# Performance work log

Hardware: AMD Instinct MI355X
Metric: run time of the kernel (lower is better)

The kernel has to match this reference:

```python
import jax, jax.numpy as jnp
import numpy as np

NU, NI, D, LAYERS, NNZ = 50000, 50000, 256, 2, 400000
N = NU + NI
LEAKY_ALPHA = 0.2  # tf.nn.leaky_relu default


def setup_inputs() -> dict:
    key = jax.random.key(0)
    ks = jax.random.split(key, 32)
    inp = {}
    inp["initial_ebs"] = jax.random.normal(ks[0], (N, D), jnp.float32) * 0.1
    for i, nm in enumerate(["W_side_u", "W_dot_u", "W_side_i", "W_dot_i"]):
        inp[nm] = jax.random.normal(ks[1 + i], (LAYERS, D, D), jnp.float32) / np.float32(np.sqrt(D))
    vi = 5
    for ent, ne in (("u", NU), ("i", NI)):
        for mat in ("LI", "L"):
            inp[f"{mat}_vals_{ent}"] = jax.random.uniform(ks[vi], (NNZ,), jnp.float32); vi += 1
            inp[f"{mat}_rows_{ent}"] = jnp.sort(jax.random.randint(ks[vi], (NNZ,), 0, ne, jnp.int32)); vi += 1
            inp[f"{mat}_cols_{ent}"] = jax.random.randint(ks[vi], (NNZ,), 0, N, jnp.int32); vi += 1
    return inp


def _spmm(rows, cols, vals, ebs, n_rows):
    # sparse [n_rows, N] @ dense [N, D] via gather + segment-sum
    return jax.ops.segment_sum(vals[:, None] * ebs[cols], rows, num_segments=n_rows)


def reference(initial_ebs, W_side_u, W_dot_u, W_side_i, W_dot_i,
              LI_vals_u, L_vals_u, LI_vals_i, L_vals_i,
              LI_rows_u, LI_cols_u, L_rows_u, L_cols_u,
              LI_rows_i, LI_cols_i, L_rows_i, L_cols_i):
    ebs = initial_ebs
    layers_ebs = []
    for l in range(LAYERS):
        # entity 'u': rows [0, NU)
        li_u = _spmm(LI_rows_u, LI_cols_u, LI_vals_u, ebs, NU)
        l_u = _spmm(L_rows_u, L_cols_u, L_vals_u, ebs, NU)
        fold_u = jax.nn.leaky_relu(li_u @ W_side_u[l] + (l_u * ebs[:NU]) @ W_dot_u[l], LEAKY_ALPHA)
        # entity 'i': rows [NU, N)
        li_i = _spmm(LI_rows_i, LI_cols_i, LI_vals_i, ebs, NI)
        l_i = _spmm(L_rows_i, L_cols_i, L_vals_i, ebs, NI)
        fold_i = jax.nn.leaky_relu(li_i @ W_side_i[l] + (l_i * ebs[NU:]) @ W_dot_i[l], LEAKY_ALPHA)
        ebs = jnp.concatenate([fold_u, fold_i], axis=0)  # [N, D]
        layers_ebs.append(ebs)
    return jnp.concatenate(layers_ebs, axis=0)  # [LAYERS*N, D]
```

## Files before the change

kernel.cpp:

```cpp
#include <hip/hip_runtime.h>

#define NUQ 50000
#define NIQ 50000
#define DQ 256
#define NTOT 100000
#define LALPHA 0.2f
#define GPE 782

typedef __attribute__((ext_vector_type(8))) __bf16 bf16x8;
typedef __attribute__((ext_vector_type(4))) float floatx4;
typedef __attribute__((ext_vector_type(8))) unsigned short ushort8;

__device__ __forceinline__ float b2f(unsigned short u) {
    unsigned int x = ((unsigned int)u) << 16;
    return __builtin_bit_cast(float, x);
}
__device__ __forceinline__ unsigned short f2b(float f) {
    unsigned int u = __builtin_bit_cast(unsigned int, f);
    u = u + 0x7FFFu + ((u >> 16) & 1u);
    return (unsigned short)(u >> 16);
}

#define GLD_LDS16(g, l)                                                        \
    __builtin_amdgcn_global_load_lds(                                          \
        (const __attribute__((address_space(1))) void*)(g),                    \
        (__attribute__((address_space(3))) void*)(l), 16, 0, 0)

__global__ __launch_bounds__(256) void build_rowptr(
    const int* __restrict__ rows, int nnz, int* __restrict__ rptr, int n_rows)
{
    int e = blockIdx.x * 256 + threadIdx.x;
    if (e > nnz) return;
    int prev = (e == 0)   ? -1     : rows[e - 1];
    int cur  = (e == nnz) ? n_rows : rows[e];
    for (int r = prev + 1; r <= cur; ++r) rptr[r] = e;
}

__global__ __launch_bounds__(256) void cvt_f32_bf16(
    const float* __restrict__ in, unsigned short* __restrict__ out, int n4)
{
    int i = blockIdx.x * 256 + threadIdx.x;
    if (i >= n4) return;
    float4 v = ((const float4*)in)[i];
    ushort4 o;
    o.x = f2b(v.x); o.y = f2b(v.y); o.z = f2b(v.z); o.w = f2b(v.w);
    ((ushort4*)out)[i] = o;
}

__global__ __launch_bounds__(256) void build_bt(
    const float* __restrict__ Ws_u, const float* __restrict__ Wd_u,
    const float* __restrict__ Ws_i, const float* __restrict__ Wd_i,
    unsigned short* __restrict__ Bt)
{
    int idx = blockIdx.x * 256 + threadIdx.x;
    int k   = idx & 511;
    int n   = (idx >> 9) & 255;
    int buf = idx >> 17;
    int l = buf >> 1, e = buf & 1;
    const float* Wside = e ? Ws_i : Ws_u;
    const float* Wdot  = e ? Wd_i : Wd_u;
    float v = (k < 256) ? Wside[((size_t)l * 256 + k)       * 256 + n]
                        : Wdot [((size_t)l * 256 + (k-256)) * 256 + n];
    Bt[idx] = f2b(v);
}

__global__ __launch_bounds__(256) void spmm_dual_v2(
    const int* __restrict__ rpA_u, const int* __restrict__ cA_u, const float* __restrict__ vA_u,
    const int* __restrict__ rpB_u, const int* __restrict__ cB_u, const float* __restrict__ vB_u,
    const int* __restrict__ rpA_i, const int* __restrict__ cA_i, const float* __restrict__ vA_i,
    const int* __restrict__ rpB_i, const int* __restrict__ cB_i, const float* __restrict__ vB_i,
    const unsigned short* __restrict__ src,
    unsigned short* __restrict__ out)
{
    const int wave = threadIdx.x >> 6;
    const int lane = threadIdx.x & 63;
    const int r    = blockIdx.x * 4 + wave;
    if (r >= NTOT) return;
    const int  isB = blockIdx.y;
    const bool isI = (r >= NUQ);
    const int  row = isI ? (r - NUQ) : r;

    const int* rptr; const int* cols; const float* vals;
    if (isB) { rptr = isI ? rpB_i : rpB_u; cols = isI ? cB_i : cB_u; vals = isI ? vB_i : vB_u; }
    else     { rptr = isI ? rpA_i : rpA_u; cols = isI ? cA_i : cA_u; vals = isI ? vA_i : vA_u; }

    const int start = rptr[row];
    const int end   = rptr[row + 1];

    const int half = lane >> 5;
    const int li   = lane & 31;

    float acc[8] = {0.f, 0.f, 0.f, 0.f, 0.f, 0.f, 0.f, 0.f};

    for (int base = start; base < end; base += 64) {
        int cnt = end - base; if (cnt > 64) cnt = 64;
        int myc = 0; float myv = 0.f;
        if (lane < cnt) { myc = cols[base + lane]; myv = vals[base + lane]; }
        #pragma unroll 2
        for (int e = 0; e < cnt; e += 2) {
            const int idx = e + half;
            const int   c = __shfl(myc, idx, 64);
            const float v = __shfl(myv, idx, 64);
            const ushort8 s = *(const ushort8*)(src + (size_t)c * DQ + li * 8);
            #pragma unroll
            for (int j = 0; j < 8; ++j) acc[j] = fmaf(v, b2f(s[j]), acc[j]);
        }
    }

    #pragma unroll
    for (int j = 0; j < 8; ++j) acc[j] += __shfl_xor(acc[j], 32, 64);

    if (half == 0) {
        if (isB) {
            const ushort8 m = *(const ushort8*)(src + (size_t)r * DQ + li * 8);
            #pragma unroll
            for (int j = 0; j < 8; ++j) acc[j] *= b2f(m[j]);
        }
        ushort8 o;
        #pragma unroll
        for (int j = 0; j < 8; ++j) o[j] = f2b(acc[j]);
        *(ushort8*)(out + (size_t)r * 512 + isB * 256 + li * 8) = o;
    }
}

__global__ __launch_bounds__(256) void gemm_mfma_leaky_v2(
    const unsigned short* __restrict__ A,
    const unsigned short* __restrict__ Btl,
    float* __restrict__ out,
    unsigned short* __restrict__ ebs,
    const int wb)
{
    __shared__ unsigned short As[2][2048];
    __shared__ unsigned short Bs[2][8192];

    const int tid  = threadIdx.x;
    const int lane = tid & 63;
    const int w    = tid >> 6;
    const int ent  = (blockIdx.x >= GPE) ? 1 : 0;
    const int bx   = blockIdx.x - ent * GPE;
    const int row0 = ent * NUQ + bx * 64;
    const int Mend = ent * NUQ + NUQ;
    const unsigned short* Bt = Btl + (size_t)ent * 131072;

    const int mA  = ((tid >> 6) << 4) | (tid & 15);
    const int kbA = (tid >> 4) & 3;
    int grs = row0 + mA; if (grs >= Mend) grs = Mend - 1;
    const unsigned short* gA = A + (size_t)grs * 512 + kbA * 8;
    const int ldsA = w * 512;

    const unsigned short* gB[4];
    #pragma unroll
    for (int j = 0; j < 4; ++j) {
        int t = j * 256 + tid;
        int n = ((t >> 6) << 4) | (t & 15);
        gB[j] = Bt + (size_t)n * 512 + ((t >> 4) & 3) * 8;
    }
    const int ldsB = w * 512;

    const int lr  = lane >> 4;
    const int lc  = lane & 15;
    const int gmb = (w & 1) * 2;
    const int gnb = (w >> 1) * 8;

    floatx4 acc[2][8] = {};

    GLD_LDS16(gA, &As[0][ldsA]);
    #pragma unroll
    for (int j = 0; j < 4; ++j)
        GLD_LDS16(gB[j], &Bs[0][j * 2048 + ldsB]);
    __syncthreads();

    int cur = 0;
    for (int kt = 0; kt < 16; ++kt) {
        if (kt < 15) {
            const int ko = (kt + 1) * 32;
            GLD_LDS16(gA + ko, &As[cur ^ 1][ldsA]);
            #pragma unroll
            for (int j = 0; j < 4; ++j)
                GLD_LDS16(gB[j] + ko, &Bs[cur ^ 1][j * 2048 + ldsB]);
        }

        bf16x8 af[2], bfr[8];
        #pragma unroll
        for (int tm = 0; tm < 2; ++tm)
            af[tm] = *(const bf16x8*)&As[cur][(gmb + tm) * 512 + lr * 128 + lc * 8];
        #pragma unroll
        for (int tn = 0; tn < 8; ++tn)
            bfr[tn] = *(const bf16x8*)&Bs[cur][(gnb + tn) * 512 + lr * 128 + lc * 8];

        #pragma unroll
        for (int tm = 0; tm < 2; ++tm)
            #pragma unroll
            for (int tn = 0; tn < 8; ++tn)
                acc[tm][tn] = __builtin_amdgcn_mfma_f32_16x16x32_bf16(
                    af[tm], bfr[tn], acc[tm][tn], 0, 0, 0);

        __syncthreads();
        cur ^= 1;
    }

    const int m_off = (w & 1) * 32;
    const int n_off = (w >> 1) * 128;
    #pragma unroll
    for (int tm = 0; tm < 2; ++tm) {
        #pragma unroll
        for (int rr = 0; rr < 4; ++rr) {
            const int gr = row0 + m_off + tm * 16 + lr * 4 + rr;
            if (gr >= Mend) continue;
            float*          orow = out + (size_t)gr * 256;
            unsigned short* brow = ebs + (size_t)gr * 256;
            #pragma unroll
            for (int tn = 0; tn < 8; ++tn) {
                const int gc = n_off + tn * 16 + lc;
                float v = acc[tm][tn][rr];
                v = v > 0.f ? v : LALPHA * v;
                orow[gc] = v;
                if (wb) brow[gc] = f2b(v);
            }
        }
    }
}

extern "C" void kernel_launch(void* const* d_in, const int* in_sizes, int n_in,
                              void* d_out, int out_size, void* d_ws, size_t ws_size,
                              hipStream_t stream) {
    const float* ebs0      = (const float*)d_in[0];
    const float* W_side_u  = (const float*)d_in[1];
    const float* W_dot_u   = (const float*)d_in[2];
    const float* W_side_i  = (const float*)d_in[3];
    const float* W_dot_i   = (const float*)d_in[4];
    const float* LI_vals_u = (const float*)d_in[5];
    const int*   LI_rows_u = (const int*)  d_in[6];
    const int*   LI_cols_u = (const int*)  d_in[7];
    const float* L_vals_u  = (const float*)d_in[8];
    const int*   L_rows_u  = (const int*)  d_in[9];
    const int*   L_cols_u  = (const int*)  d_in[10];
    const float* LI_vals_i = (const float*)d_in[11];
    const int*   LI_rows_i = (const int*)  d_in[12];
    const int*   LI_cols_i = (const int*)  d_in[13];
    const float* L_vals_i  = (const float*)d_in[14];
    const int*   L_rows_i  = (const int*)  d_in[15];
    const int*   L_cols_i  = (const int*)  d_in[16];

    float* out = (float*)d_out;

    unsigned short* Abuf   = (unsigned short*)d_ws;
    unsigned short* ebs_bf = (unsigned short*)((char*)d_ws + 102400000);
    unsigned short* Bt     = (unsigned short*)((char*)d_ws + 153600000);
    int* rp_LI_u = (int*)((char*)d_ws + 154648576);
    int* rp_L_u  = rp_LI_u + 50001;
    int* rp_LI_i = rp_L_u  + 50001;
    int* rp_L_i  = rp_LI_i + 50001;

    const int nnz_LI_u = in_sizes[5];
    const int nnz_L_u  = in_sizes[8];
    const int nnz_LI_i = in_sizes[11];
    const int nnz_L_i  = in_sizes[14];

    dim3 b256(256);
    build_rowptr<<<dim3((nnz_LI_u + 256) / 256), b256, 0, stream>>>(LI_rows_u, nnz_LI_u, rp_LI_u, NUQ);
    build_rowptr<<<dim3((nnz_L_u  + 256) / 256), b256, 0, stream>>>(L_rows_u,  nnz_L_u,  rp_L_u,  NUQ);
    build_rowptr<<<dim3((nnz_LI_i + 256) / 256), b256, 0, stream>>>(LI_rows_i, nnz_LI_i, rp_LI_i, NIQ);
    build_rowptr<<<dim3((nnz_L_i  + 256) / 256), b256, 0, stream>>>(L_rows_i,  nnz_L_i,  rp_L_i,  NIQ);
    build_bt<<<dim3(2048), b256, 0, stream>>>(W_side_u, W_dot_u, W_side_i, W_dot_i, Bt);
    cvt_f32_bf16<<<dim3(25000), b256, 0, stream>>>(ebs0, ebs_bf, NTOT * DQ / 4);

    dim3 sgrid(NTOT / 4, 2);
    dim3 ggrid(2 * GPE);

    for (int l = 0; l < 2; ++l) {
        float* outl = out + (size_t)l * NTOT * DQ;
        spmm_dual_v2<<<sgrid, b256, 0, stream>>>(
            rp_LI_u, LI_cols_u, LI_vals_u, rp_L_u, L_cols_u, L_vals_u,
            rp_LI_i, LI_cols_i, LI_vals_i, rp_L_i, L_cols_i, L_vals_i,
            ebs_bf, Abuf);
        gemm_mfma_leaky_v2<<<ggrid, b256, 0, stream>>>(
            Abuf, Bt + (size_t)l * 2 * 131072, outl, ebs_bf, (l == 0) ? 1 : 0);
    }
}
```

Baseline: 736.7 us.

## Merge dual SpMM into one wave per row and deepen GEMM prefetch pipeline

```diff
diff --git a/kernel.cpp b/kernel.cpp
--- a/kernel.cpp
+++ b/kernel.cpp
@@ -64,7 +64,7 @@
     Bt[idx] = f2b(v);
 }
 
-__global__ __launch_bounds__(256) void spmm_dual_v2(
+__global__ __launch_bounds__(256) void spmm_merged_v3(
     const int* __restrict__ rpA_u, const int* __restrict__ cA_u, const float* __restrict__ vA_u,
     const int* __restrict__ rpB_u, const int* __restrict__ cB_u, const float* __restrict__ vB_u,
     const int* __restrict__ rpA_i, const int* __restrict__ cA_i, const float* __restrict__ vA_i,
@@ -74,56 +74,76 @@
 {
     const int wave = threadIdx.x >> 6;
     const int lane = threadIdx.x & 63;
-    const int r    = blockIdx.x * 4 + wave;
-    if (r >= NTOT) return;
-    const int  isB = blockIdx.y;
+    const int r    = __builtin_amdgcn_readfirstlane(blockIdx.x * 4 + wave);
     const bool isI = (r >= NUQ);
     const int  row = isI ? (r - NUQ) : r;
 
-    const int* rptr; const int* cols; const float* vals;
-    if (isB) { rptr = isI ? rpB_i : rpB_u; cols = isI ? cB_i : cB_u; vals = isI ? vB_i : vB_u; }
-    else     { rptr = isI ? rpA_i : rpA_u; cols = isI ? cA_i : cA_u; vals = isI ? vA_i : vA_u; }
-
-    const int start = rptr[row];
-    const int end   = rptr[row + 1];
+    const int*   rpA = isI ? rpA_i : rpA_u;
+    const int*   cAp = isI ? cA_i  : cA_u;
+    const float* vAp = isI ? vA_i  : vA_u;
+    const int*   rpB = isI ? rpB_i : rpB_u;
+    const int*   cBp = isI ? cB_i  : cB_u;
+    const float* vBp = isI ? vB_i  : vB_u;
+
+    const int sA = rpA[row], eA = rpA[row + 1];
+    const int sB = rpB[row], eB = rpB[row + 1];
 
     const int half = lane >> 5;
     const int li   = lane & 31;
 
-    float acc[8] = {0.f, 0.f, 0.f, 0.f, 0.f, 0.f, 0.f, 0.f};
-
-    for (int base = start; base < end; base += 64) {
-        int cnt = end - base; if (cnt > 64) cnt = 64;
-        int myc = 0; float myv = 0.f;
-        if (lane < cnt) { myc = cols[base + lane]; myv = vals[base + lane]; }
+    float accA[8] = {0.f, 0.f, 0.f, 0.f, 0.f, 0.f, 0.f, 0.f};
+    float accB[8] = {0.f, 0.f, 0.f, 0.f, 0.f, 0.f, 0.f, 0.f};
+
+    int baseA = sA, baseB = sB;
+    while (baseA < eA || baseB < eB) {
+        int cntA = eA - baseA; cntA = cntA < 0 ? 0 : (cntA > 64 ? 64 : cntA);
+        int cntB = eB - baseB; cntB = cntB < 0 ? 0 : (cntB > 64 ? 64 : cntB);
+        int mycA = 0; float myvA = 0.f;
+        if (lane < cntA) { mycA = cAp[baseA + lane]; myvA = vAp[baseA + lane]; }
+        int mycB = 0; float myvB = 0.f;
+        if (lane < cntB) { mycB = cBp[baseB + lane]; myvB = vBp[baseB + lane]; }
+        const int mx = cntA > cntB ? cntA : cntB;
         #pragma unroll 2
-        for (int e = 0; e < cnt; e += 2) {
-            const int idx = e + half;
-            const int   c = __shfl(myc, idx, 64);
-            const float v = __shfl(myv, idx, 64);
-            const ushort8 s = *(const ushort8*)(src + (size_t)c * DQ + li * 8);
-            #pragma unroll
-            for (int j = 0; j < 8; ++j) acc[j] = fmaf(v, b2f(s[j]), acc[j]);
+        for (int e = 0; e < mx; e += 2) {
+            if (e < cntA) {
+                const int   c = __shfl(mycA, e + half, 64);
+                const float v = __shfl(myvA, e + half, 64);
+                const ushort8 s = *(const ushort8*)(src + (size_t)c * DQ + li * 8);
+                #pragma unroll
+                for (int j = 0; j < 8; ++j) accA[j] = fmaf(v, b2f(s[j]), accA[j]);
+            }
+            if (e < cntB) {
+                const int   c = __shfl(mycB, e + half, 64);
+                const float v = __shfl(myvB, e + half, 64);
+                const ushort8 s = *(const ushort8*)(src + (size_t)c * DQ + li * 8);
+                #pragma unroll
+                for (int j = 0; j < 8; ++j) accB[j] = fmaf(v, b2f(s[j]), accB[j]);
+            }
         }
-    }
-
-    #pragma unroll
-    for (int j = 0; j < 8; ++j) acc[j] += __shfl_xor(acc[j], 32, 64);
-
+        baseA += 64; baseB += 64;
+    }
+
+    #pragma unroll
+    for (int j = 0; j < 8; ++j) accA[j] += __shfl_xor(accA[j], 32, 64);
+    #pragma unroll
+    for (int j = 0; j < 8; ++j) accB[j] += __shfl_xor(accB[j], 32, 64);
+
+    float vo[8];
     if (half == 0) {
-        if (isB) {
-            const ushort8 m = *(const ushort8*)(src + (size_t)r * DQ + li * 8);
-            #pragma unroll
-            for (int j = 0; j < 8; ++j) acc[j] *= b2f(m[j]);
-        }
-        ushort8 o;
-        #pragma unroll
-        for (int j = 0; j < 8; ++j) o[j] = f2b(acc[j]);
-        *(ushort8*)(out + (size_t)r * 512 + isB * 256 + li * 8) = o;
-    }
-}
-
-__global__ __launch_bounds__(256) void gemm_mfma_leaky_v2(
+        #pragma unroll
+        for (int j = 0; j < 8; ++j) vo[j] = accA[j];
+    } else {
+        const ushort8 m = *(const ushort8*)(src + (size_t)r * DQ + li * 8);
+        #pragma unroll
+        for (int j = 0; j < 8; ++j) vo[j] = accB[j] * b2f(m[j]);
+    }
+    ushort8 o;
+    #pragma unroll
+    for (int j = 0; j < 8; ++j) o[j] = f2b(vo[j]);
+    *(ushort8*)(out + (size_t)r * 512 + half * 256 + li * 8) = o;
+}
+
+__global__ __launch_bounds__(256) void gemm_mfma_leaky_v3(
     const unsigned short* __restrict__ A,
     const unsigned short* __restrict__ Btl,
     float* __restrict__ out,
@@ -166,37 +186,44 @@
 
     GLD_LDS16(gA, &As[0][ldsA]);
     #pragma unroll
-    for (int j = 0; j < 4; ++j)
-        GLD_LDS16(gB[j], &Bs[0][j * 2048 + ldsB]);
-    __syncthreads();
-
-    int cur = 0;
+    for (int j = 0; j < 4; ++j) GLD_LDS16(gB[j], &Bs[0][j * 2048 + ldsB]);
+    GLD_LDS16(gA + 32, &As[1][ldsA]);
+    #pragma unroll
+    for (int j = 0; j < 4; ++j) GLD_LDS16(gB[j] + 32, &Bs[1][j * 2048 + ldsB]);
+
     for (int kt = 0; kt < 16; ++kt) {
-        if (kt < 15) {
-            const int ko = (kt + 1) * 32;
-            GLD_LDS16(gA + ko, &As[cur ^ 1][ldsA]);
+        const int cur = kt & 1;
+        if (kt < 15) asm volatile("s_waitcnt vmcnt(5)" ::: "memory");
+        else         asm volatile("s_waitcnt vmcnt(0)" ::: "memory");
+        __builtin_amdgcn_s_barrier();
+
+        bf16x8 af[2], bfr[8];
+        #pragma unroll
+        for (int tm = 0; tm < 2; ++tm)
+            af[tm] = *(const bf16x8*)&As[cur][(gmb + tm) * 512 + lr * 128 + lc * 8];
+        #pragma unroll
+        for (int tn = 0; tn < 8; ++tn)
+            bfr[tn] = *(const bf16x8*)&Bs[cur][(gnb + tn) * 512 + lr * 128 + lc * 8];
+
+        asm volatile("s_waitcnt lgkmcnt(0)" ::: "memory");
+        __builtin_amdgcn_s_barrier();
+
+        if (kt < 14) {
+            const int ko = (kt + 2) * 32;
+            GLD_LDS16(gA + ko, &As[cur][ldsA]);
             #pragma unroll
             for (int j = 0; j < 4; ++j)
-                GLD_LDS16(gB[j] + ko, &Bs[cur ^ 1][j * 2048 + ldsB]);
+                GLD_LDS16(gB[j] + ko, &Bs[cur][j * 2048 + ldsB]);
         }
 
-        bf16x8 af[2], bfr[8];
-        #pragma unroll
-        for (int tm = 0; tm < 2; ++tm)
-            af[tm] = *(const bf16x8*)&As[cur][(gmb + tm) * 512 + lr * 128 + lc * 8];
-        #pragma unroll
-        for (int tn = 0; tn < 8; ++tn)
-            bfr[tn] = *(const bf16x8*)&Bs[cur][(gnb + tn) * 512 + lr * 128 + lc * 8];
-
+        __builtin_amdgcn_s_setprio(1);
         #pragma unroll
         for (int tm = 0; tm < 2; ++tm)
             #pragma unroll
             for (int tn = 0; tn < 8; ++tn)
                 acc[tm][tn] = __builtin_amdgcn_mfma_f32_16x16x32_bf16(
                     af[tm], bfr[tn], acc[tm][tn], 0, 0, 0);
-
-        __syncthreads();
-        cur ^= 1;
+        __builtin_amdgcn_s_setprio(0);
     }
 
     const int m_off = (w & 1) * 32;
@@ -265,16 +292,16 @@
     build_bt<<<dim3(2048), b256, 0, stream>>>(W_side_u, W_dot_u, W_side_i, W_dot_i, Bt);
     cvt_f32_bf16<<<dim3(25000), b256, 0, stream>>>(ebs0, ebs_bf, NTOT * DQ / 4);
 
-    dim3 sgrid(NTOT / 4, 2);
+    dim3 sgrid(NTOT / 4);
     dim3 ggrid(2 * GPE);
 
     for (int l = 0; l < 2; ++l) {
         float* outl = out + (size_t)l * NTOT * DQ;
-        spmm_dual_v2<<<sgrid, b256, 0, stream>>>(
+        spmm_merged_v3<<<sgrid, b256, 0, stream>>>(
             rp_LI_u, LI_cols_u, LI_vals_u, rp_L_u, L_cols_u, L_vals_u,
             rp_LI_i, LI_cols_i, LI_vals_i, rp_L_i, L_cols_i, L_vals_i,
             ebs_bf, Abuf);
-        gemm_mfma_leaky_v2<<<ggrid, b256, 0, stream>>>(
+        gemm_mfma_leaky_v3<<<ggrid, b256, 0, stream>>>(
             Abuf, Bt + (size_t)l * 2 * 131072, outl, ebs_bf, (l == 0) ? 1 : 0);
     }
 }
```

After: 706.5 us. -4.1%, faster.
